# Optimization experiments

Measured on AMD Instinct MI355X. Metric: run time of the kernel, lower is better.

## Reference

```python
import jax, jax.numpy as jnp
import numpy as np


def setup_inputs() -> dict:
    key = jax.random.key(0)
    ks = jax.random.split(key, 8)
    T, A, F, H, N, E = 64, 64, 512, 1024, 512, 4
    s1, s2, s3 = 1.0 / np.sqrt(F), 1.0 / np.sqrt(H), 1.0 / np.sqrt(H)
    return {
        "obs": jax.random.normal(ks[0], (T, A, F), dtype=jnp.float32),
        "W1": jax.random.normal(ks[1], (E, F, H), dtype=jnp.float32) * s1,
        "b1": jnp.zeros((E, H), dtype=jnp.float32),
        "W2": jax.random.normal(ks[2], (E, H, H), dtype=jnp.float32) * s2,
        "b2": jnp.zeros((E, H), dtype=jnp.float32),
        "W3": jax.random.normal(ks[3], (E, H, N), dtype=jnp.float32) * s3,
        "b3": jnp.zeros((E, N), dtype=jnp.float32),
        "agent_type": jax.random.randint(ks[4], (T, A), 0, E, dtype=jnp.int32),
    }


def reference(obs, W1, b1, W2, b2, W3, b3, agent_type):
    # distribute_compute: for each type e, gather obs[mask_e], run expert e's
    # MLP, scatter logits back into a zero-init (T, A, n_action) buffer.
    # Dense-equivalent form: run every expert on all tokens, then select the
    # row belonging to each agent's type (masks partition agents, so the
    # zero-init scatter == one-hot select).
    E = W1.shape[0]
    h = jax.nn.relu(jnp.einsum('taf,efh->etah', obs, W1) + b1[:, None, None, :])
    h = jax.nn.relu(jnp.einsum('etah,ehg->etag', h, W2) + b2[:, None, None, :])
    y = jnp.einsum('etah,ehn->etan', h, W3) + b3[:, None, None, :]  # (E,T,A,N)
    sel = jax.nn.one_hot(agent_type, E, dtype=y.dtype)              # (T,A,E)
    out = jnp.einsum('etan,tae->tan', y, sel)                       # (T,A,N)
    return out
```

## Files before the change

### kernel.cpp

```cpp
#include <hip/hip_runtime.h>
#include <stdint.h>

#define T_DIM 64
#define A_DIM 64
#define F_DIM 512
#define H_DIM 1024
#define N_DIM 512
#define E_DIM 4
#define NTOK 4096
#define NTOK_PAD 4224
#define NSLOT 72

typedef __attribute__((ext_vector_type(8))) short short8;
typedef __attribute__((ext_vector_type(4))) short short4v;
typedef __attribute__((ext_vector_type(4))) float f32x4;

__device__ __forceinline__ unsigned short f2bf(float x) {
  unsigned u = __float_as_uint(x);
  u += 0x7fffu + ((u >> 16) & 1u);
  return (unsigned short)(u >> 16);
}
__device__ __forceinline__ float bf2f(unsigned short h) {
  return __uint_as_float(((unsigned)h) << 16);
}
__device__ __forceinline__ void split_bf(float x, short& hi, short& lo) {
  unsigned short h = f2bf(x);
  hi = (short)h;
  lo = (short)f2bf(x - bf2f(h));
}

__device__ __forceinline__ void gload_lds16(const void* g, void* l) {
  __builtin_amdgcn_global_load_lds(
      (const __attribute__((address_space(1))) unsigned int*)g,
      (__attribute__((address_space(3))) unsigned int*)l, 16, 0, 0);
}

__global__ __launch_bounds__(1024) void k_route(const int* __restrict__ at,
                                                int* __restrict__ pos,
                                                int4* __restrict__ slots) {
  __shared__ int wt[16][4];
  __shared__ int woff[16][4];
  __shared__ int soff[4];
  int tid = threadIdx.x;
  int w = tid >> 6, ln = tid & 63;

  int4 a = ((const int4*)at)[tid];
  int c[4] = {0, 0, 0, 0};
  c[a.x]++; c[a.y]++; c[a.z]++; c[a.w]++;

  int inc[4];
#pragma unroll
  for (int e = 0; e < 4; ++e) inc[e] = c[e];
#pragma unroll
  for (int d = 1; d < 64; d <<= 1) {
#pragma unroll
    for (int e = 0; e < 4; ++e) {
      int u = __shfl_up(inc[e], d, 64);
      if (ln >= d) inc[e] += u;
    }
  }
  if (ln == 63) {
#pragma unroll
    for (int e = 0; e < 4; ++e) wt[w][e] = inc[e];
  }
  __syncthreads();
  if (tid == 0) {
    int tot[4] = {0, 0, 0, 0};
    for (int i = 0; i < 16; ++i)
      for (int e = 0; e < 4; ++e) { woff[i][e] = tot[e]; tot[e] += wt[i][e]; }
    int acc = 0;
    int sbase[4];
    for (int e = 0; e < 4; ++e) { sbase[e] = acc; soff[e] = acc; acc += tot[e]; }
    int si = 0;
    for (int e = 0; e < 4; ++e) {
      int cnt = tot[e];
      for (int m = 0; m * 64 < cnt; ++m) {
        int4 s;
        s.x = sbase[e] + m * 64;
        s.y = (cnt - m * 64) < 64 ? (cnt - m * 64) : 64;
        s.z = e; s.w = 0;
        slots[si++] = s;
      }
    }
    int4 z; z.x = 0; z.y = 0; z.z = 0; z.w = 0;
    while (si < NSLOT) slots[si++] = z;
  }
  __syncthreads();
  int excl[4];
#pragma unroll
  for (int e = 0; e < 4; ++e) excl[e] = soff[e] + woff[w][e] + inc[e] - c[e];
  int es[4] = {a.x, a.y, a.z, a.w};
#pragma unroll
  for (int k = 0; k < 4; ++k) {
    int e = es[k];
    pos[tid * 4 + k] = excl[e];
    excl[e]++;
  }
}

__global__ void k_gather(const float* __restrict__ obs, const int* __restrict__ pos,
                         int* __restrict__ idx,
                         short* __restrict__ oH, short* __restrict__ oL) {
  int tid = threadIdx.x;
  int t = blockIdx.x * 4 + (tid >> 6);
  int ln = tid & 63;
  int p = pos[t];
  if (ln == 0) idx[p] = t;
  const float* src = obs + (size_t)t * F_DIM;
  int base = ln * 8;
  float4 v0 = *(const float4*)(src + base);
  float4 v1 = *(const float4*)(src + base + 4);
  float xs[8] = {v0.x, v0.y, v0.z, v0.w, v1.x, v1.y, v1.z, v1.w};
  short8 hh, ll;
#pragma unroll
  for (int i = 0; i < 8; ++i) {
    short h, l;
    split_bf(xs[i], h, l);
    hh[i] = h; ll[i] = l;
  }
  *(short8*)&oH[(size_t)p * F_DIM + base] = hh;
  *(short8*)&oL[(size_t)p * F_DIM + base] = ll;
}

__global__ void k_wsplit(const float* __restrict__ W, short* __restrict__ Th,
                         short* __restrict__ Tl, int K, int N) {
  int e  = blockIdx.z;
  int n0 = blockIdx.x * 64;
  int k0 = blockIdx.y * 64;
  __shared__ float tile[64][65];
  const float* w = W + (size_t)e * K * N;
  int tr = threadIdx.x >> 4;
  int tc = threadIdx.x & 15;
#pragma unroll
  for (int i = 0; i < 4; ++i) {
    int kk = k0 + i * 16 + tr;
    float4 v = *(const float4*)(w + (size_t)kk * N + n0 + tc * 4);
    tile[i * 16 + tr][tc * 4 + 0] = v.x;
    tile[i * 16 + tr][tc * 4 + 1] = v.y;
    tile[i * 16 + tr][tc * 4 + 2] = v.z;
    tile[i * 16 + tr][tc * 4 + 3] = v.w;
  }
  __syncthreads();
#pragma unroll
  for (int i = 0; i < 4; ++i) {
    int nr = i * 16 + tr;
    size_t ob = ((size_t)e * N + (n0 + nr)) * K + k0 + tc * 4;
    short4v hh, ll;
#pragma unroll
    for (int j = 0; j < 4; ++j) {
      float x = tile[tc * 4 + j][nr];
      short h, l;
      split_bf(x, h, l);
      hh[j] = h; ll[j] = l;
    }
    *(short4v*)&Th[ob] = hh;
    *(short4v*)&Tl[ob] = ll;
  }
}

template <int K, int NOUT, bool RELU, bool FINAL>
__launch_bounds__(256, 3)
__global__ void k_gemm(const short* __restrict__ Ah, const short* __restrict__ Al,
                       const short* __restrict__ Bh, const short* __restrict__ Bl,
                       const float* __restrict__ bias,
                       short* __restrict__ Ch, short* __restrict__ Cl,
                       float* __restrict__ outF, const int* __restrict__ idx,
                       const int4* __restrict__ slots) {
  constexpr int NT  = NOUT / 128;
  constexpr int NWG = NSLOT * NT;
  int wg   = (blockIdx.x & 7) * (NWG / 8) + (blockIdx.x >> 3);
  int slot = wg / NT;
  int nt   = wg % NT;
  int4 s = slots[slot];
  int rows = s.y;
  if (rows == 0) return;
  int row0 = s.x, e = s.z, row_end = row0 + rows;
  int ncol0 = nt * 128;

  __shared__ short lds[2][12288];

  int tid = threadIdx.x, wave = tid >> 6, ln = tid & 63;
  const short* bPh = Bh + (size_t)e * NOUT * K;
  const short* bPl = Bl + (size_t)e * NOUT * K;

  const short* srcb[6];
#pragma unroll
  for (int r = 0; r < 6; ++r) {
    int g = r * 256 + tid;
    if (g < 256)       { int wc = g;        srcb[r] = Ah  + (size_t)(row0  + (wc >> 2)) * K + (wc & 3) * 8; }
    else if (g < 512)  { int wc = g - 256;  srcb[r] = Al  + (size_t)(row0  + (wc >> 2)) * K + (wc & 3) * 8; }
    else if (g < 1024) { int wc = g - 512;  srcb[r] = bPh + (size_t)(ncol0 + (wc >> 2)) * K + (wc & 3) * 8; }
    else               { int wc = g - 1024; srcb[r] = bPl + (size_t)(ncol0 + (wc >> 2)) * K + (wc & 3) * 8; }
  }

  int wbase = (tid & ~63) * 8;

  auto stage = [&](int buf, int ks) {
    int k0 = ks * 32;
#pragma unroll
    for (int r = 0; r < 6; ++r)
      gload_lds16(srcb[r] + k0, (void*)&lds[buf][r * 2048 + wbase]);
  };

  f32x4 acc[2][4] = {};
  int wr = wave >> 1, wcn = wave & 1;
  int tm = ln & 15, kg = ln >> 4;

  stage(0, 0);
  __syncthreads();
  constexpr int NK = K / 32;
  for (int ks = 0; ks < NK; ++ks) {
    int cb = ks & 1;
    if (ks + 1 < NK) stage(cb ^ 1, ks + 1);
    short8 ah[2], al[2], bh[4], bl[4];
#pragma unroll
    for (int i = 0; i < 2; ++i) {
      int ar = (wr * 32 + i * 16 + tm) * 32 + kg * 8;
      ah[i] = *(const short8*)&lds[cb][ar];
      al[i] = *(const short8*)&lds[cb][2048 + ar];
    }
#pragma unroll
    for (int j = 0; j < 4; ++j) {
      int br = (wcn * 64 + j * 16 + tm) * 32 + kg * 8;
      bh[j] = *(const short8*)&lds[cb][4096 + br];
      bl[j] = *(const short8*)&lds[cb][8192 + br];
    }
#pragma unroll
    for (int i = 0; i < 2; ++i)
#pragma unroll
      for (int j = 0; j < 4; ++j) {
        acc[i][j] = __builtin_amdgcn_mfma_f32_16x16x32_bf16(ah[i], bh[j], acc[i][j], 0, 0, 0);
        acc[i][j] = __builtin_amdgcn_mfma_f32_16x16x32_bf16(ah[i], bl[j], acc[i][j], 0, 0, 0);
        acc[i][j] = __builtin_amdgcn_mfma_f32_16x16x32_bf16(al[i], bh[j], acc[i][j], 0, 0, 0);
      }
    __syncthreads();
  }

  int lcol = ln & 15;
  int lrow4 = (ln >> 4) * 4;
#pragma unroll
  for (int j = 0; j < 4; ++j) {
    int col = ncol0 + wcn * 64 + j * 16 + lcol;
    float bv = bias[(size_t)e * NOUT + col];
#pragma unroll
    for (int i = 0; i < 2; ++i) {
      int gr0 = row0 + wr * 32 + i * 16 + lrow4;
#pragma unroll
      for (int q = 0; q < 4; ++q) {
        int grow = gr0 + q;
        if (grow < row_end) {
          float x = acc[i][j][q] + bv;
          if (RELU) x = fmaxf(x, 0.0f);
          if (FINAL) {
            int token = idx[grow];
            outF[(size_t)token * NOUT + col] = x;
          } else {
            short h, l;
            split_bf(x, h, l);
            Ch[(size_t)grow * NOUT + col] = h;
            Cl[(size_t)grow * NOUT + col] = l;
          }
        }
      }
    }
  }
}

extern "C" void kernel_launch(void* const* d_in, const int* in_sizes, int n_in,
                              void* d_out, int out_size, void* d_ws, size_t ws_size,
                              hipStream_t stream) {
  (void)in_sizes; (void)n_in; (void)out_size; (void)ws_size;
  const float* obs = (const float*)d_in[0];
  const float* W1  = (const float*)d_in[1];
  const float* b1  = (const float*)d_in[2];
  const float* W2  = (const float*)d_in[3];
  const float* b2  = (const float*)d_in[4];
  const float* W3  = (const float*)d_in[5];
  const float* b3  = (const float*)d_in[6];
  const int*   at  = (const int*)d_in[7];
  float* out = (float*)d_out;

  char* w = (char*)d_ws;
  auto carve = [&](size_t bytes) {
    char* p = w;
    w += (bytes + 255) & ~(size_t)255;
    return p;
  };
  int*  pos   = (int*)carve(NTOK * 4);
  int4* slots = (int4*)carve(NSLOT * 16);
  int*  idx   = (int*)carve(NTOK_PAD * 4);
  short* obsH = (short*)carve((size_t)NTOK_PAD * F_DIM * 2);
  short* obsL = (short*)carve((size_t)NTOK_PAD * F_DIM * 2);
  short* h1H  = (short*)carve((size_t)NTOK_PAD * H_DIM * 2);
  short* h1L  = (short*)carve((size_t)NTOK_PAD * H_DIM * 2);
  short* h2H  = (short*)carve((size_t)NTOK_PAD * H_DIM * 2);
  short* h2L  = (short*)carve((size_t)NTOK_PAD * H_DIM * 2);
  short* w1h  = (short*)carve((size_t)E_DIM * H_DIM * F_DIM * 2);
  short* w1l  = (short*)carve((size_t)E_DIM * H_DIM * F_DIM * 2);
  short* w2h  = (short*)carve((size_t)E_DIM * H_DIM * H_DIM * 2);
  short* w2l  = (short*)carve((size_t)E_DIM * H_DIM * H_DIM * 2);
  short* w3h  = (short*)carve((size_t)E_DIM * N_DIM * H_DIM * 2);
  short* w3l  = (short*)carve((size_t)E_DIM * N_DIM * H_DIM * 2);

  k_route<<<1, 1024, 0, stream>>>(at, pos, slots);
  k_gather<<<NTOK / 4, 256, 0, stream>>>(obs, pos, idx, obsH, obsL);

  k_wsplit<<<dim3(H_DIM / 64, F_DIM / 64, E_DIM), 256, 0, stream>>>(W1, w1h, w1l, F_DIM, H_DIM);
  k_wsplit<<<dim3(H_DIM / 64, H_DIM / 64, E_DIM), 256, 0, stream>>>(W2, w2h, w2l, H_DIM, H_DIM);
  k_wsplit<<<dim3(N_DIM / 64, H_DIM / 64, E_DIM), 256, 0, stream>>>(W3, w3h, w3l, H_DIM, N_DIM);

  k_gemm<F_DIM, H_DIM, true, false>
      <<<NSLOT * (H_DIM / 128), 256, 0, stream>>>(
          obsH, obsL, w1h, w1l, b1, h1H, h1L, nullptr, nullptr, slots);
  k_gemm<H_DIM, H_DIM, true, false>
      <<<NSLOT * (H_DIM / 128), 256, 0, stream>>>(
          h1H, h1L, w2h, w2l, b2, h2H, h2L, nullptr, nullptr, slots);
  k_gemm<H_DIM, N_DIM, false, true>
      <<<NSLOT * (N_DIM / 128), 256, 0, stream>>>(
          h2H, h2L, w3h, w3l, b3, nullptr, nullptr, out, idx, slots);
}
```

Baseline: 215.6 us.

## Triple-buffer GEMM LDS with swizzle and merge prep kernels into one launch

The GEMM moves from a double-buffered LDS pipeline to a three-stage one. It keeps two tiles in flight, waits with an explicit vmcnt and uses raw barriers, and it XOR-swizzles the LDS chunk layout to cut bank conflicts on fragment reads. The gather and the three weight-split kernels become one launch, which removes launch gaps and lets those blocks run concurrently. Triple buffering raises LDS use per block, so occupancy drops (launch bounds go from 3 to 2 blocks) in exchange for better latency hiding.

After: 219.7 us. Within noise of the previous version (+1.9%).

```diff
diff --git a/kernel.cpp b/kernel.cpp
--- a/kernel.cpp
+++ b/kernel.cpp
@@ -98,36 +98,11 @@
   }
 }
 
-__global__ void k_gather(const float* __restrict__ obs, const int* __restrict__ pos,
-                         int* __restrict__ idx,
-                         short* __restrict__ oH, short* __restrict__ oL) {
-  int tid = threadIdx.x;
-  int t = blockIdx.x * 4 + (tid >> 6);
-  int ln = tid & 63;
-  int p = pos[t];
-  if (ln == 0) idx[p] = t;
-  const float* src = obs + (size_t)t * F_DIM;
-  int base = ln * 8;
-  float4 v0 = *(const float4*)(src + base);
-  float4 v1 = *(const float4*)(src + base + 4);
-  float xs[8] = {v0.x, v0.y, v0.z, v0.w, v1.x, v1.y, v1.z, v1.w};
-  short8 hh, ll;
-#pragma unroll
-  for (int i = 0; i < 8; ++i) {
-    short h, l;
-    split_bf(xs[i], h, l);
-    hh[i] = h; ll[i] = l;
-  }
-  *(short8*)&oH[(size_t)p * F_DIM + base] = hh;
-  *(short8*)&oL[(size_t)p * F_DIM + base] = ll;
-}
-
-__global__ void k_wsplit(const float* __restrict__ W, short* __restrict__ Th,
-                         short* __restrict__ Tl, int K, int N) {
-  int e  = blockIdx.z;
-  int n0 = blockIdx.x * 64;
-  int k0 = blockIdx.y * 64;
-  __shared__ float tile[64][65];
+__device__ __forceinline__ void wsplit_tile(const float* __restrict__ W,
+                                            short* __restrict__ Th,
+                                            short* __restrict__ Tl,
+                                            int K, int N, int e, int n0, int k0,
+                                            float (*tile)[65]) {
   const float* w = W + (size_t)e * K * N;
   int tr = threadIdx.x >> 4;
   int tc = threadIdx.x & 15;
@@ -158,8 +133,54 @@
   }
 }
 
+__global__ __launch_bounds__(256) void k_prep(
+    const float* __restrict__ obs, const int* __restrict__ pos, int* __restrict__ idx,
+    short* __restrict__ oH, short* __restrict__ oL,
+    const float* __restrict__ W1, short* __restrict__ w1h, short* __restrict__ w1l,
+    const float* __restrict__ W2, short* __restrict__ w2h, short* __restrict__ w2l,
+    const float* __restrict__ W3, short* __restrict__ w3h, short* __restrict__ w3l) {
+  __shared__ float tile[64][65];
+  int b = blockIdx.x;
+  if (b < 1024) {
+    int tid = threadIdx.x;
+    int t = b * 4 + (tid >> 6);
+    int ln = tid & 63;
+    int p = pos[t];
+    if (ln == 0) idx[p] = t;
+    const float* src = obs + (size_t)t * F_DIM;
+    int base = ln * 8;
+    float4 v0 = *(const float4*)(src + base);
+    float4 v1 = *(const float4*)(src + base + 4);
+    float xs[8] = {v0.x, v0.y, v0.z, v0.w, v1.x, v1.y, v1.z, v1.w};
+    short8 hh, ll;
+#pragma unroll
+    for (int i = 0; i < 8; ++i) {
+      short h, l;
+      split_bf(xs[i], h, l);
+      hh[i] = h; ll[i] = l;
+    }
+    *(short8*)&oH[(size_t)p * F_DIM + base] = hh;
+    *(short8*)&oL[(size_t)p * F_DIM + base] = ll;
+  } else if (b < 1536) {
+    int i = b - 1024;
+    int e = i >> 7, r = i & 127;
+    int n0 = (r >> 3) * 64, k0 = (r & 7) * 64;
+    wsplit_tile(W1, w1h, w1l, F_DIM, H_DIM, e, n0, k0, tile);
+  } else if (b < 2560) {
+    int i = b - 1536;
+    int e = i >> 8, r = i & 255;
+    int n0 = (r >> 4) * 64, k0 = (r & 15) * 64;
+    wsplit_tile(W2, w2h, w2l, H_DIM, H_DIM, e, n0, k0, tile);
+  } else {
+    int i = b - 2560;
+    int e = i >> 7, r = i & 127;
+    int n0 = (r >> 4) * 64, k0 = (r & 15) * 64;
+    wsplit_tile(W3, w3h, w3l, H_DIM, N_DIM, e, n0, k0, tile);
+  }
+}
+
 template <int K, int NOUT, bool RELU, bool FINAL>
-__launch_bounds__(256, 3)
+__launch_bounds__(256, 2)
 __global__ void k_gemm(const short* __restrict__ Ah, const short* __restrict__ Al,
                        const short* __restrict__ Bh, const short* __restrict__ Bl,
                        const float* __restrict__ bias,
@@ -177,7 +198,7 @@
   int row0 = s.x, e = s.z, row_end = row0 + rows;
   int ncol0 = nt * 128;
 
-  __shared__ short lds[2][12288];
+  __shared__ short lds[3][12288];
 
   int tid = threadIdx.x, wave = tid >> 6, ln = tid & 63;
   const short* bPh = Bh + (size_t)e * NOUT * K;
@@ -187,10 +208,14 @@
 #pragma unroll
   for (int r = 0; r < 6; ++r) {
     int g = r * 256 + tid;
-    if (g < 256)       { int wc = g;        srcb[r] = Ah  + (size_t)(row0  + (wc >> 2)) * K + (wc & 3) * 8; }
-    else if (g < 512)  { int wc = g - 256;  srcb[r] = Al  + (size_t)(row0  + (wc >> 2)) * K + (wc & 3) * 8; }
-    else if (g < 1024) { int wc = g - 512;  srcb[r] = bPh + (size_t)(ncol0 + (wc >> 2)) * K + (wc & 3) * 8; }
-    else               { int wc = g - 1024; srcb[r] = bPl + (size_t)(ncol0 + (wc >> 2)) * K + (wc & 3) * 8; }
+    const short* plane; int wc, rb;
+    if (g < 256)       { plane = Ah;  wc = g;        rb = row0;  }
+    else if (g < 512)  { plane = Al;  wc = g - 256;  rb = row0;  }
+    else if (g < 1024) { plane = bPh; wc = g - 512;  rb = ncol0; }
+    else               { plane = bPl; wc = g - 1024; rb = ncol0; }
+    int prow = wc >> 2;
+    int lch  = (wc & 3) ^ ((wc >> 3) & 3);
+    srcb[r] = plane + (size_t)(rb + prow) * K + lch * 8;
   }
 
   int wbase = (tid & ~63) * 8;
@@ -206,24 +231,41 @@
   int wr = wave >> 1, wcn = wave & 1;
   int tm = ln & 15, kg = ln >> 4;
 
+  int aoff[2], boff[4];
+#pragma unroll
+  for (int i = 0; i < 2; ++i) {
+    int arow = wr * 32 + i * 16 + tm;
+    aoff[i] = arow * 32 + (kg ^ ((arow >> 1) & 3)) * 8;
+  }
+#pragma unroll
+  for (int j = 0; j < 4; ++j) {
+    int brow = wcn * 64 + j * 16 + tm;
+    boff[j] = brow * 32 + (kg ^ ((brow >> 1) & 3)) * 8;
+  }
+
   stage(0, 0);
-  __syncthreads();
+  stage(1, 1);
   constexpr int NK = K / 32;
+  int cb = 0, sb = 2;
   for (int ks = 0; ks < NK; ++ks) {
-    int cb = ks & 1;
-    if (ks + 1 < NK) stage(cb ^ 1, ks + 1);
+    if (ks < NK - 1) {
+      asm volatile("s_waitcnt vmcnt(6)" ::: "memory");
+    } else {
+      asm volatile("s_waitcnt vmcnt(0)" ::: "memory");
+    }
+    __builtin_amdgcn_s_barrier();
+    asm volatile("" ::: "memory");
+
     short8 ah[2], al[2], bh[4], bl[4];
 #pragma unroll
     for (int i = 0; i < 2; ++i) {
-      int ar = (wr * 32 + i * 16 + tm) * 32 + kg * 8;
-      ah[i] = *(const short8*)&lds[cb][ar];
-      al[i] = *(const short8*)&lds[cb][2048 + ar];
+      ah[i] = *(const short8*)&lds[cb][aoff[i]];
+      al[i] = *(const short8*)&lds[cb][2048 + aoff[i]];
     }
 #pragma unroll
     for (int j = 0; j < 4; ++j) {
-      int br = (wcn * 64 + j * 16 + tm) * 32 + kg * 8;
-      bh[j] = *(const short8*)&lds[cb][4096 + br];
-      bl[j] = *(const short8*)&lds[cb][8192 + br];
+      bh[j] = *(const short8*)&lds[cb][4096 + boff[j]];
+      bl[j] = *(const short8*)&lds[cb][8192 + boff[j]];
     }
 #pragma unroll
     for (int i = 0; i < 2; ++i)
@@ -233,7 +275,13 @@
         acc[i][j] = __builtin_amdgcn_mfma_f32_16x16x32_bf16(ah[i], bl[j], acc[i][j], 0, 0, 0);
         acc[i][j] = __builtin_amdgcn_mfma_f32_16x16x32_bf16(al[i], bh[j], acc[i][j], 0, 0, 0);
       }
-    __syncthreads();
+
+    asm volatile("" ::: "memory");
+    __builtin_amdgcn_s_barrier();
+    asm volatile("" ::: "memory");
+    if (ks + 2 < NK) stage(sb, ks + 2);
+    cb = (cb == 2) ? 0 : cb + 1;
+    sb = (sb == 2) ? 0 : sb + 1;
   }
 
   int lcol = ln & 15;
@@ -303,11 +351,8 @@
   short* w3l  = (short*)carve((size_t)E_DIM * N_DIM * H_DIM * 2);
 
   k_route<<<1, 1024, 0, stream>>>(at, pos, slots);
-  k_gather<<<NTOK / 4, 256, 0, stream>>>(obs, pos, idx, obsH, obsL);
-
-  k_wsplit<<<dim3(H_DIM / 64, F_DIM / 64, E_DIM), 256, 0, stream>>>(W1, w1h, w1l, F_DIM, H_DIM);
-  k_wsplit<<<dim3(H_DIM / 64, H_DIM / 64, E_DIM), 256, 0, stream>>>(W2, w2h, w2l, H_DIM, H_DIM);
-  k_wsplit<<<dim3(N_DIM / 64, H_DIM / 64, E_DIM), 256, 0, stream>>>(W3, w3h, w3l, H_DIM, N_DIM);
+  k_prep<<<3072, 256, 0, stream>>>(obs, pos, idx, obsH, obsL,
+                                   W1, w1h, w1l, W2, w2h, w2l, W3, w3h, w3l);
 
   k_gemm<F_DIM, H_DIM, true, false>
       <<<NSLOT * (H_DIM / 128), 256, 0, stream>>>(
```
